# Optimization experiments

Measured on AMD Instinct MI355X. Metric: run time of the kernel, lower is better.

Reference implementation:

```python
import jax, jax.numpy as jnp
import numpy as np

D = 512        # feat_dim
H_ENC = 8      # motion_encoder heads
H_SA = 4       # semantic-aware attention heads
BS, L, N = 8, 512, 4096
LN_EPS = 1e-5


def _layernorm(x, g, b):
    m = jnp.mean(x, axis=-1, keepdims=True)
    v = jnp.var(x, axis=-1, keepdims=True)
    return (x - m) * jax.lax.rsqrt(v + LN_EPS) * g + b


def _linear(x, w, b):
    # torch nn.Linear convention: w [out, in]
    return x @ w.T + b


def setup_inputs() -> dict:
    key = jax.random.key(0)
    ks = jax.random.split(key, 24)
    s = 0.02
    inp = {
        "motion": jax.random.normal(ks[0], (BS, L, D), jnp.float32),
        "scene_xyz": jax.random.normal(ks[1], (BS, N, 3), jnp.float32),
        "scene_feats": jax.random.normal(ks[2], (BS, N, D), jnp.float32),
        "spatial_prior": jax.random.normal(ks[3], (BS, L, N), jnp.float32),
        # motion_encoder (pre-norm MHA + pre-norm MLP, both residual)
        "enc_ln1_g": jnp.ones((D,), jnp.float32),
        "enc_ln1_b": jnp.zeros((D,), jnp.float32),
        "enc_qkv_w": jax.random.normal(ks[4], (3 * D, D), jnp.float32) * s,
        "enc_qkv_b": jnp.zeros((3 * D,), jnp.float32),
        "enc_out_w": jax.random.normal(ks[5], (D, D), jnp.float32) * s,
        "enc_out_b": jnp.zeros((D,), jnp.float32),
        "enc_ln2_g": jnp.ones((D,), jnp.float32),
        "enc_ln2_b": jnp.zeros((D,), jnp.float32),
        "enc_ff1_w": jax.random.normal(ks[6], (D, D), jnp.float32) * s,
        "enc_ff1_b": jnp.zeros((D,), jnp.float32),
        "enc_ff2_w": jax.random.normal(ks[7], (D, D), jnp.float32) * s,
        "enc_ff2_b": jnp.zeros((D,), jnp.float32),
        # SemanticAwareAttention
        "sa_q_w": jax.random.normal(ks[8], (D, D), jnp.float32) * s,
        "sa_q_b": jnp.zeros((D,), jnp.float32),
        "sa_kv_w": jax.random.normal(ks[9], (2 * D, D), jnp.float32) * s,
        "sa_kv_b": jnp.zeros((2 * D,), jnp.float32),
        "sa_out_w": jax.random.normal(ks[10], (D, D), jnp.float32) * s,
        "sa_out_b": jnp.zeros((D,), jnp.float32),
        # final concat-MLP: in 2D -> 4D -> D  (Mlp(2D, D, expansion=4))
        "mlp_fc1_w": jax.random.normal(ks[11], (4 * D, 2 * D), jnp.float32) * s,
        "mlp_fc1_b": jnp.zeros((4 * D,), jnp.float32),
        "mlp_fc2_w": jax.random.normal(ks[12], (D, 4 * D), jnp.float32) * s,
        "mlp_fc2_b": jnp.zeros((D,), jnp.float32),
    }
    return inp


def _forward(motion, scene_xyz, scene_feats, spatial_prior,
             enc_ln1_g, enc_ln1_b, enc_qkv_w, enc_qkv_b, enc_out_w, enc_out_b,
             enc_ln2_g, enc_ln2_b, enc_ff1_w, enc_ff1_b, enc_ff2_w, enc_ff2_b,
             sa_q_w, sa_q_b, sa_kv_w, sa_kv_b, sa_out_w, sa_out_b,
             mlp_fc1_w, mlp_fc1_b, mlp_fc2_w, mlp_fc2_b):
    bs, slen, _ = motion.shape
    n = scene_feats.shape[1]
    dh_enc = D // H_ENC
    dh_sa = D // H_SA

    # ---- motion encoder: pre-norm MHA + residual ----
    h = _layernorm(motion, enc_ln1_g, enc_ln1_b)
    qkv = _linear(h, enc_qkv_w, enc_qkv_b)                      # [bs, L, 3D]
    q, k, v = jnp.split(qkv, 3, axis=-1)
    q = q.reshape(bs, slen, H_ENC, dh_enc)
    k = k.reshape(bs, slen, H_ENC, dh_enc)
    v = v.reshape(bs, slen, H_ENC, dh_enc)
    att = jnp.einsum("bqhd,bkhd->bhqk", q, k) * (dh_enc ** -0.5)
    att = jax.nn.softmax(att, axis=-1)
    o = jnp.einsum("bhqk,bkhd->bqhd", att, v).reshape(bs, slen, D)
    x = motion + _linear(o, enc_out_w, enc_out_b)

    # ---- pre-norm MLP + residual ----
    h2 = _layernorm(x, enc_ln2_g, enc_ln2_b)
    ff = _linear(jax.nn.gelu(_linear(h2, enc_ff1_w, enc_ff1_b), approximate=False),
                 enc_ff2_w, enc_ff2_b)
    motion_sca = x + ff

    # ---- SemanticAwareAttention ----
    q = _linear(motion_sca, sa_q_w, sa_q_b) * (D ** -0.5)       # scale by feat_dim (faithful)
    kv = _linear(scene_feats, sa_kv_w, sa_kv_b)
    k, v = jnp.split(kv, 2, axis=-1)
    # faithful to torch: q.view(bs, H, L, d) splits heads from flattened (L, D)
    q = q.reshape(bs, H_SA, slen, dh_sa)
    k = k.reshape(bs, n, H_SA, dh_sa).transpose(0, 2, 1, 3)     # [bs, H, N, d]
    v = v.reshape(bs, n, H_SA, dh_sa).transpose(0, 2, 1, 3)
    att = jnp.einsum("bhqd,bhkd->bhqk", q, k) + spatial_prior[:, None, :, :]
    att = jax.nn.softmax(att, axis=-1)
    sm = jnp.einsum("bhqk,bhkd->bqhd", att, v).reshape(bs, slen, D)
    sm_feature = _linear(sm, sa_out_w, sa_out_b)

    # ---- concat + MLP ----
    cat = jnp.concatenate([motion_sca, sm_feature], axis=-1)    # [bs, L, 2D]
    out = _linear(jax.nn.gelu(_linear(cat, mlp_fc1_w, mlp_fc1_b), approximate=False),
                  mlp_fc2_w, mlp_fc2_b)
    return out


def reference(motion, scene_xyz, scene_feats, spatial_prior,
              enc_ln1_g, enc_ln1_b, enc_qkv_w, enc_qkv_b, enc_out_w, enc_out_b,
              enc_ln2_g, enc_ln2_b, enc_ff1_w, enc_ff1_b, enc_ff2_w, enc_ff2_b,
              sa_q_w, sa_q_b, sa_kv_w, sa_kv_b, sa_out_w, sa_out_b,
              mlp_fc1_w, mlp_fc1_b, mlp_fc2_w, mlp_fc2_b):
    return _forward(motion, scene_xyz, scene_feats, spatial_prior,
                    enc_ln1_g, enc_ln1_b, enc_qkv_w, enc_qkv_b, enc_out_w, enc_out_b,
                    enc_ln2_g, enc_ln2_b, enc_ff1_w, enc_ff1_b, enc_ff2_w, enc_ff2_b,
                    sa_q_w, sa_q_b, sa_kv_w, sa_kv_b, sa_out_w, sa_out_b,
                    mlp_fc1_w, mlp_fc1_b, mlp_fc2_w, mlp_fc2_b)
```

## Files before the change

### kernel.cpp

```cpp
#include <hip/hip_runtime.h>

typedef unsigned short bf16_t;
typedef __attribute__((ext_vector_type(8))) short bf16x8;
typedef __attribute__((ext_vector_type(4))) float f32x4;

__device__ __forceinline__ float bf2f(bf16_t u) {
  union { unsigned int i; float f; } v; v.i = ((unsigned int)u) << 16; return v.f;
}
__device__ __forceinline__ bf16_t f2bf(float f) {
  union { float f; unsigned int i; } v; v.f = f;
  unsigned int u = v.i;
  u += 0x7fffu + ((u >> 16) & 1u);
  return (bf16_t)(u >> 16);
}
__device__ __forceinline__ float gelu_exact(float x) {
  return 0.5f * x * (1.0f + erff(x * 0.7071067811865475f));
}

__global__ __launch_bounds__(256) void f2bf_kernel(const float4* __restrict__ s,
                                                   ushort4* __restrict__ d, int n4) {
  int i = blockIdx.x * 256 + threadIdx.x;
  if (i < n4) {
    float4 f = s[i];
    ushort4 u; u.x = f2bf(f.x); u.y = f2bf(f.y); u.z = f2bf(f.z); u.w = f2bf(f.w);
    d[i] = u;
  }
}

__global__ __launch_bounds__(256) void ln_kernel(const float* __restrict__ x,
                                                 const float* __restrict__ g,
                                                 const float* __restrict__ bta,
                                                 bf16_t* __restrict__ y) {
  const int w = threadIdx.x >> 6, lane = threadIdx.x & 63;
  const long row = (long)blockIdx.x * 4 + w;
  const long base = row * 512;
  const int c0 = lane << 2;
  float v[8];
  float4 f0 = *(const float4*)(x + base + c0);
  float4 f1 = *(const float4*)(x + base + 256 + c0);
  v[0]=f0.x; v[1]=f0.y; v[2]=f0.z; v[3]=f0.w;
  v[4]=f1.x; v[5]=f1.y; v[6]=f1.z; v[7]=f1.w;
  float s = 0.f;
#pragma unroll
  for (int c=0;c<8;++c) s += v[c];
#pragma unroll
  for (int o=32;o>0;o>>=1) s += __shfl_xor(s, o);
  const float mean = s * 0.001953125f;
  float ss = 0.f;
#pragma unroll
  for (int c=0;c<8;++c) { float d = v[c]-mean; ss += d*d; }
#pragma unroll
  for (int o=32;o>0;o>>=1) ss += __shfl_xor(ss, o);
  const float rstd = rsqrtf(ss * 0.001953125f + 1e-5f);
  ushort4 o0, o1;
  o0.x = f2bf((v[0]-mean)*rstd*g[c0+0] + bta[c0+0]);
  o0.y = f2bf((v[1]-mean)*rstd*g[c0+1] + bta[c0+1]);
  o0.z = f2bf((v[2]-mean)*rstd*g[c0+2] + bta[c0+2]);
  o0.w = f2bf((v[3]-mean)*rstd*g[c0+3] + bta[c0+3]);
  o1.x = f2bf((v[4]-mean)*rstd*g[256+c0+0] + bta[256+c0+0]);
  o1.y = f2bf((v[5]-mean)*rstd*g[256+c0+1] + bta[256+c0+1]);
  o1.z = f2bf((v[6]-mean)*rstd*g[256+c0+2] + bta[256+c0+2]);
  o1.w = f2bf((v[7]-mean)*rstd*g[256+c0+3] + bta[256+c0+3]);
  *(ushort4*)(y + base + c0) = o0;
  *(ushort4*)(y + base + 256 + c0) = o1;
}

struct MmaNT {
  const bf16_t* A; const bf16_t* W; const float* bias; const float* res; void* C;
  long lda, sAb, sAh;
  long ldw, sWb, sWh;
  long ldr, sRb, sRh;
  long ldc, sCb, sCh;
  int K, zdiv, cBf, act;
  float scale;
};

template <int MT>
__global__ __launch_bounds__(256) void mma_nt_kernel(MmaNT p) {
  constexpr int FM = MT / 32;
  __shared__ __align__(16) bf16_t smem[MT * 128];
  const int tid = threadIdx.x;
  const int wid = tid >> 6, lane = tid & 63;
  const int wm = wid & 1, wn = wid >> 1;
  const int quad = lane >> 4, l16 = lane & 15;
  const int z = blockIdx.z;
  const int zb = z / p.zdiv, zh = z % p.zdiv;

  const int nbx = gridDim.x;
  const int nwg = nbx * gridDim.y;
  const int flat = blockIdx.y * nbx + blockIdx.x;
  const int sw = (flat & 7) * (nwg >> 3) + (flat >> 3);
  const int bx = sw % nbx, by = sw / nbx;

  const long m0 = (long)by * MT;
  const long n0 = (long)bx * 128;
  const bf16_t* Ag = p.A + (long)zb * p.sAb + (long)zh * p.sAh +
                     (m0 + wm * (MT / 2) + l16) * p.lda;
  const bf16_t* Wg = p.W + (long)zb * p.sWb + (long)zh * p.sWh +
                     (n0 + wn * 64 + l16) * p.ldw;

  f32x4 zero4 = {0.f, 0.f, 0.f, 0.f};
  f32x4 acc[FM][4];
#pragma unroll
  for (int fm = 0; fm < FM; ++fm)
#pragma unroll
    for (int fn = 0; fn < 4; ++fn) acc[fm][fn] = zero4;

  bf16x8 af[FM], wf[4];
#pragma unroll
  for (int fm = 0; fm < FM; ++fm)
    af[fm] = *(const bf16x8*)(Ag + (long)(fm * 16) * p.lda + quad * 8);
#pragma unroll
  for (int fn = 0; fn < 4; ++fn)
    wf[fn] = *(const bf16x8*)(Wg + (long)(fn * 16) * p.ldw + quad * 8);

  for (int kc = 0; kc < p.K; kc += 32) {
    bf16x8 afn[FM], wfn[4];
    const int kn = kc + 32;
    if (kn < p.K) {
#pragma unroll
      for (int fm = 0; fm < FM; ++fm)
        afn[fm] = *(const bf16x8*)(Ag + (long)(fm * 16) * p.lda + kn + quad * 8);
#pragma unroll
      for (int fn = 0; fn < 4; ++fn)
        wfn[fn] = *(const bf16x8*)(Wg + (long)(fn * 16) * p.ldw + kn + quad * 8);
    }
#pragma unroll
    for (int fm = 0; fm < FM; ++fm)
#pragma unroll
      for (int fn = 0; fn < 4; ++fn)
        acc[fm][fn] = __builtin_amdgcn_mfma_f32_16x16x32_bf16(af[fm], wf[fn], acc[fm][fn], 0, 0, 0);
#pragma unroll
    for (int fm = 0; fm < FM; ++fm) af[fm] = afn[fm];
#pragma unroll
    for (int fn = 0; fn < 4; ++fn) wf[fn] = wfn[fn];
  }

  const long cOff = (long)zb * p.sCb + (long)zh * p.sCh;
  const long rOff = (long)zb * p.sRb + (long)zh * p.sRh;
  if (p.cBf) {
#pragma unroll
    for (int fm = 0; fm < FM; ++fm) {
#pragma unroll
      for (int fn = 0; fn < 4; ++fn) {
        const int lc = wn * 64 + fn * 16 + l16;
        const long col = n0 + lc;
        const float bv = p.bias ? p.bias[col] : 0.f;
#pragma unroll
        for (int r = 0; r < 4; ++r) {
          const int lr = wm * (MT / 2) + fm * 16 + quad * 4 + r;
          float t = acc[fm][fn][r] + bv;
          if (p.act) t = gelu_exact(t);
          t *= p.scale;
          if (p.res) t += p.res[rOff + (m0 + lr) * p.ldr + col];
          smem[lr * 128 + lc] = f2bf(t);
        }
      }
    }
    __syncthreads();
    bf16_t* Cg = (bf16_t*)p.C + cOff + m0 * p.ldc + n0;
#pragma unroll
    for (int i = 0; i < MT / 16; ++i) {
      const int flat2 = tid + i * 256;
      const int r = flat2 >> 4, c = (flat2 & 15) * 8;
      *(uint4*)(Cg + (long)r * p.ldc + c) = *(const uint4*)&smem[r * 128 + c];
    }
  } else {
#pragma unroll
    for (int fm = 0; fm < FM; ++fm) {
#pragma unroll
      for (int fn = 0; fn < 4; ++fn) {
        const long col = n0 + wn * 64 + fn * 16 + l16;
        const float bv = p.bias ? p.bias[col] : 0.f;
#pragma unroll
        for (int r = 0; r < 4; ++r) {
          const long row = m0 + wm * (MT / 2) + fm * 16 + quad * 4 + r;
          float t = acc[fm][fn][r] + bv;
          if (p.act) t = gelu_exact(t);
          t *= p.scale;
          if (p.res) t += p.res[rOff + row * p.ldr + col];
          ((float*)p.C)[cOff + row * p.ldc + col] = t;
        }
      }
    }
  }
}

struct TransP {
  const bf16_t* src; bf16_t* dst;
  long sSb, sSh, ld;
  int nh, N, D;
};

__global__ __launch_bounds__(256) void transpose_kernel(TransP p) {
  __shared__ bf16_t T[64][72];
  const int tid = threadIdx.x;
  const int z = blockIdx.z;
  const int zb = z / p.nh, zh = z % p.nh;
  const long n0 = (long)blockIdx.x * 64;
  const long d0 = (long)blockIdx.y * 64;
  const bf16_t* src = p.src + (long)zb * p.sSb + (long)zh * p.sSh;
  bf16_t* dst = p.dst + (long)z * p.D * p.N;
#pragma unroll
  for (int i = 0; i < 2; ++i) {
    int flat = tid + i * 256, r = flat >> 3, cg = flat & 7;
    uint4 v = *(const uint4*)(src + (n0 + r) * p.ld + d0 + cg * 8);
    *(uint4*)&T[r][cg * 8] = v;
  }
  __syncthreads();
#pragma unroll
  for (int i = 0; i < 2; ++i) {
    int flat = tid + i * 256, dr = flat >> 3, ncg = flat & 7;
    uint4 o;
    unsigned int* op = (unsigned int*)&o;
#pragma unroll
    for (int j = 0; j < 4; ++j)
      op[j] = (unsigned int)T[ncg * 8 + 2 * j][dr] | ((unsigned int)T[ncg * 8 + 2 * j + 1][dr] << 16);
    *(uint4*)(dst + (d0 + dr) * p.N + n0 + ncg * 8) = o;
  }
}

struct FlashP2 {
  const bf16_t* Q; const bf16_t* K; const bf16_t* VT; const float* prior;
  float* partO; float* partML;
  long ldq, sQb, sQh;
  long ldk, sKb, sKh;
  long sVz, sPb;
  int nh, N, segN;
  float scale;
};

template <int DH, int HASP>
__global__ __launch_bounds__(256) void flash3_kernel(FlashP2 p) {
  constexpr int KK = DH / 32;
  constexpr int NFO = DH / 16;
  constexpr int KPAD = DH + 8;
  __shared__ bf16_t Kl[64 * KPAD];
  __shared__ bf16_t Vl[DH * 72];
  __shared__ bf16_t Pl[128 * 72];
  const int tid = threadIdx.x;
  const int w = tid >> 6, lane = tid & 63;
  const int quad = lane >> 4, l16 = lane & 15;
  const int z = blockIdx.z;
  const int zb = z / p.nh, zh = z % p.nh;
  const int qr0 = blockIdx.y * 128 + w * 32;
  const bf16_t* Q = p.Q + (long)zb * p.sQb + (long)zh * p.sQh + (long)qr0 * p.ldq;
  const bf16_t* K = p.K + (long)zb * p.sKb + (long)zh * p.sKh;
  const bf16_t* VT = p.VT + (long)z * p.sVz;

  bf16x8 qf[2][KK];
#pragma unroll
  for (int fm = 0; fm < 2; ++fm)
#pragma unroll
    for (int kk = 0; kk < KK; ++kk)
      qf[fm][kk] = *(const bf16x8*)(Q + (long)(fm * 16 + l16) * p.ldq + kk * 32 + quad * 8);

  f32x4 zero4 = {0.f, 0.f, 0.f, 0.f};
  f32x4 O[2][NFO];
  float m_[2][4], l_[2][4];
#pragma unroll
  for (int fm = 0; fm < 2; ++fm) {
#pragma unroll
    for (int f = 0; f < NFO; ++f) O[fm][f] = zero4;
#pragma unroll
    for (int r = 0; r < 4; ++r) { m_[fm][r] = -1e30f; l_[fm][r] = 0.f; }
  }

  const int k0 = blockIdx.x * p.segN;
  for (int kt = k0; kt < k0 + p.segN; kt += 64) {
    __syncthreads();
    constexpr int KTH = DH / 8;
#pragma unroll
    for (int i = 0; i < DH / 32; ++i) {
      int flat = tid + i * 256, r = flat / KTH, c = (flat % KTH) * 8;
      *(uint4*)&Kl[r * KPAD + c] = *(const uint4*)(K + (long)(kt + r) * p.ldk + c);
    }
#pragma unroll
    for (int i = 0; i < DH / 32; ++i) {
      int flat = tid + i * 256, r = flat >> 3, c = (flat & 7) * 8;
      *(uint4*)&Vl[r * 72 + c] = *(const uint4*)(VT + (long)r * p.N + kt + c);
    }
    float pr[2][4][4];
    if (HASP) {
#pragma unroll
      for (int fm = 0; fm < 2; ++fm) {
        const float* PR = p.prior + (long)zb * p.sPb +
                          (long)(qr0 + fm * 16 + quad * 4) * p.N + kt;
#pragma unroll
        for (int nf = 0; nf < 4; ++nf)
#pragma unroll
          for (int r = 0; r < 4; ++r)
            pr[fm][nf][r] = PR[(long)r * p.N + nf * 16 + l16];
      }
    }
    __syncthreads();
    f32x4 s[2][4];
#pragma unroll
    for (int nf = 0; nf < 4; ++nf) { s[0][nf] = zero4; s[1][nf] = zero4; }
#pragma unroll
    for (int nf = 0; nf < 4; ++nf)
#pragma unroll
      for (int kk = 0; kk < KK; ++kk) {
        bf16x8 kf = *(const bf16x8*)&Kl[(nf * 16 + l16) * KPAD + kk * 32 + quad * 8];
        s[0][nf] = __builtin_amdgcn_mfma_f32_16x16x32_bf16(qf[0][kk], kf, s[0][nf], 0, 0, 0);
        s[1][nf] = __builtin_amdgcn_mfma_f32_16x16x32_bf16(qf[1][kk], kf, s[1][nf], 0, 0, 0);
      }
    float tm[2][4];
#pragma unroll
    for (int fm = 0; fm < 2; ++fm) {
#pragma unroll
      for (int r = 0; r < 4; ++r) tm[fm][r] = -1e30f;
#pragma unroll
      for (int nf = 0; nf < 4; ++nf)
#pragma unroll
        for (int r = 0; r < 4; ++r) {
          float t = s[fm][nf][r] * p.scale;
          if (HASP) t += pr[fm][nf][r];
          s[fm][nf][r] = t;
          tm[fm][r] = fmaxf(tm[fm][r], t);
        }
    }
#pragma unroll
    for (int off = 1; off < 16; off <<= 1)
#pragma unroll
      for (int fm = 0; fm < 2; ++fm)
#pragma unroll
        for (int r = 0; r < 4; ++r) tm[fm][r] = fmaxf(tm[fm][r], __shfl_xor(tm[fm][r], off));
    float alpha[2][4], rs[2][4];
#pragma unroll
    for (int fm = 0; fm < 2; ++fm)
#pragma unroll
      for (int r = 0; r < 4; ++r) {
        float mn = fmaxf(m_[fm][r], tm[fm][r]);
        alpha[fm][r] = __expf(m_[fm][r] - mn);
        m_[fm][r] = mn;
        rs[fm][r] = 0.f;
      }
#pragma unroll
    for (int fm = 0; fm < 2; ++fm)
#pragma unroll
      for (int nf = 0; nf < 4; ++nf)
#pragma unroll
        for (int r = 0; r < 4; ++r) {
          float pv = __expf(s[fm][nf][r] - m_[fm][r]);
          s[fm][nf][r] = pv;
          rs[fm][r] += pv;
        }
#pragma unroll
    for (int off = 1; off < 16; off <<= 1)
#pragma unroll
      for (int fm = 0; fm < 2; ++fm)
#pragma unroll
        for (int r = 0; r < 4; ++r) rs[fm][r] += __shfl_xor(rs[fm][r], off);
#pragma unroll
    for (int fm = 0; fm < 2; ++fm)
#pragma unroll
      for (int r = 0; r < 4; ++r) l_[fm][r] = l_[fm][r] * alpha[fm][r] + rs[fm][r];
#pragma unroll
    for (int fm = 0; fm < 2; ++fm)
#pragma unroll
      for (int nf = 0; nf < 4; ++nf)
#pragma unroll
        for (int r = 0; r < 4; ++r)
          Pl[(w * 32 + fm * 16 + quad * 4 + r) * 72 + nf * 16 + l16] = f2bf(s[fm][nf][r]);
#pragma unroll
    for (int fm = 0; fm < 2; ++fm)
#pragma unroll
      for (int f = 0; f < NFO; ++f)
#pragma unroll
        for (int r = 0; r < 4; ++r) O[fm][f][r] *= alpha[fm][r];
    bf16x8 pf[2][2];
#pragma unroll
    for (int fm = 0; fm < 2; ++fm)
#pragma unroll
      for (int kk2 = 0; kk2 < 2; ++kk2)
        pf[fm][kk2] = *(const bf16x8*)&Pl[(w * 32 + fm * 16 + l16) * 72 + kk2 * 32 + quad * 8];
#pragma unroll
    for (int f = 0; f < NFO; ++f)
#pragma unroll
      for (int kk2 = 0; kk2 < 2; ++kk2) {
        bf16x8 vf = *(const bf16x8*)&Vl[(f * 16 + l16) * 72 + kk2 * 32 + quad * 8];
        O[0][f] = __builtin_amdgcn_mfma_f32_16x16x32_bf16(pf[0][kk2], vf, O[0][f], 0, 0, 0);
        O[1][f] = __builtin_amdgcn_mfma_f32_16x16x32_bf16(pf[1][kk2], vf, O[1][f], 0, 0, 0);
      }
  }
  const long t = ((long)z * gridDim.y + blockIdx.y) * gridDim.x + blockIdx.x;
  float* PO = p.partO + t * (128 * DH);
  float* PM = p.partML + t * 256;
#pragma unroll
  for (int fm = 0; fm < 2; ++fm) {
#pragma unroll
    for (int f = 0; f < NFO; ++f)
#pragma unroll
      for (int r = 0; r < 4; ++r)
        PO[(long)(w * 32 + fm * 16 + quad * 4 + r) * DH + f * 16 + l16] = O[fm][f][r];
    if (l16 == 0) {
#pragma unroll
      for (int r = 0; r < 4; ++r) {
        PM[(w * 32 + fm * 16 + quad * 4 + r) * 2 + 0] = m_[fm][r];
        PM[(w * 32 + fm * 16 + quad * 4 + r) * 2 + 1] = l_[fm][r];
      }
    }
  }
}

struct MergeP {
  const float* partO; const float* partML; bf16_t* C;
  long ldc, sCb;
  int nh, y;
};

template <int DH, int NS>
__global__ __launch_bounds__(256) void fmerge_kernel(MergeP p) {
  const int tid = threadIdx.x;
  const int r = tid >> 1, ch = tid & 1;
  const int blk = blockIdx.x;
  const int z = blk / p.y, qb = blk % p.y;
  const int zb = z / p.nh, zh = z % p.nh;
  const long t0 = (long)blk * NS;
  float mm[NS], wgt[NS];
  float mstar = -1e30f;
#pragma unroll
  for (int s = 0; s < NS; ++s) {
    mm[s] = p.partML[(t0 + s) * 256 + r * 2];
    mstar = fmaxf(mstar, mm[s]);
  }
  float lsum = 0.f;
#pragma unroll
  for (int s = 0; s < NS; ++s) {
    wgt[s] = __expf(mm[s] - mstar);
    lsum += wgt[s] * p.partML[(t0 + s) * 256 + r * 2 + 1];
  }
  const float inv = 1.0f / lsum;
  const int c0 = ch * (DH / 2);
  bf16_t* Cp = p.C + (long)zb * p.sCb + (long)(qb * 128 + r) * p.ldc + (long)zh * DH + c0;
#pragma unroll
  for (int c = 0; c < DH / 2; c += 4) {
    float4 acc = make_float4(0.f, 0.f, 0.f, 0.f);
#pragma unroll
    for (int s = 0; s < NS; ++s) {
      float4 v = *(const float4*)(p.partO + (t0 + s) * (128 * DH) + (long)r * DH + c0 + c);
      acc.x += wgt[s] * v.x; acc.y += wgt[s] * v.y;
      acc.z += wgt[s] * v.z; acc.w += wgt[s] * v.w;
    }
    ushort4 o;
    o.x = f2bf(acc.x * inv); o.y = f2bf(acc.y * inv);
    o.z = f2bf(acc.z * inv); o.w = f2bf(acc.w * inv);
    *(ushort4*)(Cp + c) = o;
  }
}

#define MB(x) ((long)(x) << 20)

extern "C" void kernel_launch(void* const* d_in, const int* in_sizes, int n_in,
                              void* d_out, int out_size, void* d_ws, size_t ws_size,
                              hipStream_t stream) {
  const float* motion      = (const float*)d_in[0];
  const float* scene_feats = (const float*)d_in[2];
  const float* prior       = (const float*)d_in[3];
  const float* ln1_g = (const float*)d_in[4];
  const float* ln1_b = (const float*)d_in[5];
  const float* qkv_w = (const float*)d_in[6];
  const float* qkv_b = (const float*)d_in[7];
  const float* out_w = (const float*)d_in[8];
  const float* out_b = (const float*)d_in[9];
  const float* ln2_g = (const float*)d_in[10];
  const float* ln2_b = (const float*)d_in[11];
  const float* ff1_w = (const float*)d_in[12];
  const float* ff1_b = (const float*)d_in[13];
  const float* ff2_w = (const float*)d_in[14];
  const float* ff2_b = (const float*)d_in[15];
  const float* saq_w = (const float*)d_in[16];
  const float* saq_b = (const float*)d_in[17];
  const float* sakv_w = (const float*)d_in[18];
  const float* sakv_b = (const float*)d_in[19];
  const float* saout_w = (const float*)d_in[20];
  const float* saout_b = (const float*)d_in[21];
  const float* fc1_w = (const float*)d_in[22];
  const float* fc1_b = (const float*)d_in[23];
  const float* fc2_w = (const float*)d_in[24];
  const float* fc2_b = (const float*)d_in[25];

  char* W = (char*)d_ws;
  bf16_t* h_bf    = (bf16_t*)(W + MB(0));
  float*  x_f     = (float*) (W + MB(4));
  bf16_t* o_ff    = (bf16_t*)(W + MB(12));
  bf16_t* qkv_bf  = (bf16_t*)(W + MB(16));
  bf16_t* qsa     = (bf16_t*)(W + MB(28));
  bf16_t* sm_bf   = (bf16_t*)(W + MB(32));
  bf16_t* cat_bf  = (bf16_t*)(W + MB(36));
  bf16_t* fc1g    = (bf16_t*)(W + MB(44));
  bf16_t* vTe     = (bf16_t*)(W + MB(60));
  bf16_t* kv_bf   = (bf16_t*)(W + MB(64));
  bf16_t* vT      = (bf16_t*)(W + MB(128));
  bf16_t* wbase   = (bf16_t*)(W + MB(160));
  bf16_t* scene_bf= (bf16_t*)(W + MB(172));

  float* encO  = (float*)fc1g;
  float* encML = (float*)cat_bf;
  float* saO   = (float*)scene_bf;
  float* saML  = (float*)vTe;

  bf16_t* wq   = wbase + 0L;
  bf16_t* wout = wbase + 786432L;
  bf16_t* wff1 = wbase + 1048576L;
  bf16_t* wff2 = wbase + 1310720L;
  bf16_t* wsaq = wbase + 1572864L;
  bf16_t* wskv = wbase + 1835008L;
  bf16_t* wsout= wbase + 2359296L;
  bf16_t* wfc1 = wbase + 2621440L;
  bf16_t* wfc2 = wbase + 4718592L;

  const dim3 B256(256);
  auto cvt = [&](const float* s, bf16_t* d, long n) {
    int n4 = (int)(n / 4);
    f2bf_kernel<<<(n4 + 255) / 256, B256, 0, stream>>>((const float4*)s, (ushort4*)d, n4);
  };
  cvt(qkv_w,  wq,   786432);
  cvt(out_w,  wout, 262144);
  cvt(ff1_w,  wff1, 262144);
  cvt(ff2_w,  wff2, 262144);
  cvt(saq_w,  wsaq, 262144);
  cvt(sakv_w, wskv, 524288);
  cvt(saout_w,wsout,262144);
  cvt(fc1_w,  wfc1, 2097152);
  cvt(fc2_w,  wfc2, 1048576);
  cvt(scene_feats, scene_bf, 16777216);

  ln_kernel<<<1024, B256, 0, stream>>>(motion, ln1_g, ln1_b, h_bf);

  { MmaNT p{}; p.scale=1.f; p.zdiv=1; p.cBf=1;
    p.A=h_bf; p.lda=512; p.W=wq; p.ldw=512; p.bias=qkv_b;
    p.C=qkv_bf; p.ldc=1536; p.K=512;
    mma_nt_kernel<128><<<dim3(12,32,1), B256, 0, stream>>>(p); }

  { TransP t{}; t.src=qkv_bf+1024; t.dst=vTe; t.sSb=786432; t.sSh=64;
    t.ld=1536; t.nh=8; t.N=512; t.D=64;
    transpose_kernel<<<dim3(8,1,64), B256, 0, stream>>>(t); }
  { FlashP2 p{};
    p.Q=qkv_bf;     p.ldq=1536; p.sQb=786432; p.sQh=64;
    p.K=qkv_bf+512; p.ldk=1536; p.sKb=786432; p.sKh=64;
    p.VT=vTe; p.sVz=32768;
    p.prior=nullptr; p.sPb=0;
    p.partO=encO; p.partML=encML;
    p.nh=8; p.N=512; p.segN=256; p.scale=0.125f;
    flash3_kernel<64,0><<<dim3(2,4,64), B256, 0, stream>>>(p); }
  { MergeP m{}; m.partO=encO; m.partML=encML; m.C=o_ff;
    m.ldc=512; m.sCb=262144; m.nh=8; m.y=4;
    fmerge_kernel<64,2><<<256, B256, 0, stream>>>(m); }

  { MmaNT p{}; p.scale=1.f; p.zdiv=1;
    p.A=o_ff; p.lda=512; p.W=wout; p.ldw=512; p.bias=out_b;
    p.res=motion; p.ldr=512;
    p.C=x_f; p.ldc=512; p.K=512;
    mma_nt_kernel<64><<<dim3(4,64,1), B256, 0, stream>>>(p); }

  ln_kernel<<<1024, B256, 0, stream>>>(x_f, ln2_g, ln2_b, h_bf);

  { MmaNT p{}; p.scale=1.f; p.zdiv=1; p.cBf=1; p.act=1;
    p.A=h_bf; p.lda=512; p.W=wff1; p.ldw=512; p.bias=ff1_b;
    p.C=o_ff; p.ldc=512; p.K=512;
    mma_nt_kernel<64><<<dim3(4,64,1), B256, 0, stream>>>(p); }

  { MmaNT p{}; p.scale=1.f; p.zdiv=1; p.cBf=1;
    p.A=o_ff; p.lda=512; p.W=wff2; p.ldw=512; p.bias=ff2_b;
    p.res=x_f; p.ldr=512;
    p.C=cat_bf; p.ldc=1024; p.K=512;
    mma_nt_kernel<64><<<dim3(4,64,1), B256, 0, stream>>>(p); }

  { MmaNT p{}; p.zdiv=1; p.cBf=1; p.scale=0.04419417382415922f;
    p.A=cat_bf; p.lda=1024; p.W=wsaq; p.ldw=512; p.bias=saq_b;
    p.C=qsa; p.ldc=512; p.K=512;
    mma_nt_kernel<64><<<dim3(4,64,1), B256, 0, stream>>>(p); }

  { MmaNT p{}; p.scale=1.f; p.zdiv=1; p.cBf=1;
    p.A=scene_bf; p.lda=512; p.W=wskv; p.ldw=512; p.bias=sakv_b;
    p.C=kv_bf; p.ldc=1024; p.K=512;
    mma_nt_kernel<128><<<dim3(8,256,1), B256, 0, stream>>>(p); }

  { TransP t{}; t.src=kv_bf+512; t.dst=vT; t.sSb=4194304; t.sSh=128;
    t.ld=1024; t.nh=4; t.N=4096; t.D=128;
    transpose_kernel<<<dim3(64,2,32), B256, 0, stream>>>(t); }
  { FlashP2 p{};
    p.Q=qsa;   p.ldq=128;  p.sQb=262144;  p.sQh=65536;
    p.K=kv_bf; p.ldk=1024; p.sKb=4194304; p.sKh=128;
    p.VT=vT; p.sVz=524288;
    p.prior=prior; p.sPb=2097152;
    p.partO=saO; p.partML=saML;
    p.nh=4; p.N=4096; p.segN=1024; p.scale=1.f;
    flash3_kernel<128,1><<<dim3(4,4,32), B256, 0, stream>>>(p); }
  { MergeP m{}; m.partO=saO; m.partML=saML; m.C=sm_bf;
    m.ldc=512; m.sCb=262144; m.nh=4; m.y=4;
    fmerge_kernel<128,4><<<128, B256, 0, stream>>>(m); }

  { MmaNT p{}; p.scale=1.f; p.zdiv=1; p.cBf=1;
    p.A=sm_bf; p.lda=512; p.W=wsout; p.ldw=512; p.bias=saout_b;
    p.C=cat_bf + 512; p.ldc=1024; p.K=512;
    mma_nt_kernel<64><<<dim3(4,64,1), B256, 0, stream>>>(p); }

  { MmaNT p{}; p.scale=1.f; p.zdiv=1; p.cBf=1; p.act=1;
    p.A=cat_bf; p.lda=1024; p.W=wfc1; p.ldw=1024; p.bias=fc1_b;
    p.C=fc1g; p.ldc=2048; p.K=1024;
    mma_nt_kernel<128><<<dim3(16,32,1), B256, 0, stream>>>(p); }

  { MmaNT p{}; p.scale=1.f; p.zdiv=1;
    p.A=fc1g; p.lda=2048; p.W=wfc2; p.ldw=2048; p.bias=fc2_b;
    p.C=d_out; p.ldc=512; p.K=2048;
    mma_nt_kernel<64><<<dim3(4,64,1), B256, 0, stream>>>(p); }
}
```

Before: 801.6 us.

## Halve flash attention query tile to 64 rows and alias P onto K smem

Each flash block now handles 64 query rows (16 per wave) instead of 128, which doubles the grid in the y dimension and halves the per-thread accumulator and score registers. The P staging buffer now reuses the K shared-memory region, with an extra barrier before P is written, so each block needs less LDS. The merge kernel is retuned to 64-row partials with four threads per row. The intent is higher occupancy and more blocks for the long-sequence semantic-aware attention. The cost is that K/V tiles are loaded once per 64 query rows instead of per 128, doubling K/V traffic, plus one extra sync per iteration.

```diff
diff --git a/kernel.cpp b/kernel.cpp
--- a/kernel.cpp
+++ b/kernel.cpp
@@ -235,36 +235,32 @@
   constexpr int KK = DH / 32;
   constexpr int NFO = DH / 16;
   constexpr int KPAD = DH + 8;
-  __shared__ bf16_t Kl[64 * KPAD];
-  __shared__ bf16_t Vl[DH * 72];
-  __shared__ bf16_t Pl[128 * 72];
+  __shared__ bf16_t smem[64 * KPAD + DH * 72];
+  bf16_t* Kl = smem;
+  bf16_t* Pl = smem;
+  bf16_t* Vl = smem + 64 * KPAD;
   const int tid = threadIdx.x;
   const int w = tid >> 6, lane = tid & 63;
   const int quad = lane >> 4, l16 = lane & 15;
   const int z = blockIdx.z;
   const int zb = z / p.nh, zh = z % p.nh;
-  const int qr0 = blockIdx.y * 128 + w * 32;
+  const int qr0 = blockIdx.y * 64 + w * 16;
   const bf16_t* Q = p.Q + (long)zb * p.sQb + (long)zh * p.sQh + (long)qr0 * p.ldq;
   const bf16_t* K = p.K + (long)zb * p.sKb + (long)zh * p.sKh;
   const bf16_t* VT = p.VT + (long)z * p.sVz;
 
-  bf16x8 qf[2][KK];
-#pragma unroll
-  for (int fm = 0; fm < 2; ++fm)
-#pragma unroll
-    for (int kk = 0; kk < KK; ++kk)
-      qf[fm][kk] = *(const bf16x8*)(Q + (long)(fm * 16 + l16) * p.ldq + kk * 32 + quad * 8);
+  bf16x8 qf[KK];
+#pragma unroll
+  for (int kk = 0; kk < KK; ++kk)
+    qf[kk] = *(const bf16x8*)(Q + (long)l16 * p.ldq + kk * 32 + quad * 8);
 
   f32x4 zero4 = {0.f, 0.f, 0.f, 0.f};
-  f32x4 O[2][NFO];
-  float m_[2][4], l_[2][4];
-#pragma unroll
-  for (int fm = 0; fm < 2; ++fm) {
-#pragma unroll
-    for (int f = 0; f < NFO; ++f) O[fm][f] = zero4;
-#pragma unroll
-    for (int r = 0; r < 4; ++r) { m_[fm][r] = -1e30f; l_[fm][r] = 0.f; }
-  }
+  f32x4 O[NFO];
+  float m_[4], l_[4];
+#pragma unroll
+  for (int f = 0; f < NFO; ++f) O[f] = zero4;
+#pragma unroll
+  for (int r = 0; r < 4; ++r) { m_[r] = -1e30f; l_[r] = 0.f; }
 
   const int k0 = blockIdx.x * p.segN;
   for (int kt = k0; kt < k0 + p.segN; kt += 64) {
@@ -280,126 +276,101 @@
       int flat = tid + i * 256, r = flat >> 3, c = (flat & 7) * 8;
       *(uint4*)&Vl[r * 72 + c] = *(const uint4*)(VT + (long)r * p.N + kt + c);
     }
-    float pr[2][4][4];
+    float pr[4][4];
     if (HASP) {
-#pragma unroll
-      for (int fm = 0; fm < 2; ++fm) {
-        const float* PR = p.prior + (long)zb * p.sPb +
-                          (long)(qr0 + fm * 16 + quad * 4) * p.N + kt;
-#pragma unroll
-        for (int nf = 0; nf < 4; ++nf)
-#pragma unroll
-          for (int r = 0; r < 4; ++r)
-            pr[fm][nf][r] = PR[(long)r * p.N + nf * 16 + l16];
-      }
+      const float* PR = p.prior + (long)zb * p.sPb +
+                        (long)(qr0 + quad * 4) * p.N + kt;
+#pragma unroll
+      for (int nf = 0; nf < 4; ++nf)
+#pragma unroll
+        for (int r = 0; r < 4; ++r)
+          pr[nf][r] = PR[(long)r * p.N + nf * 16 + l16];
     }
     __syncthreads();
-    f32x4 s[2][4];
-#pragma unroll
-    for (int nf = 0; nf < 4; ++nf) { s[0][nf] = zero4; s[1][nf] = zero4; }
+    f32x4 s[4];
+#pragma unroll
+    for (int nf = 0; nf < 4; ++nf) s[nf] = zero4;
 #pragma unroll
     for (int nf = 0; nf < 4; ++nf)
 #pragma unroll
       for (int kk = 0; kk < KK; ++kk) {
         bf16x8 kf = *(const bf16x8*)&Kl[(nf * 16 + l16) * KPAD + kk * 32 + quad * 8];
-        s[0][nf] = __builtin_amdgcn_mfma_f32_16x16x32_bf16(qf[0][kk], kf, s[0][nf], 0, 0, 0);
-        s[1][nf] = __builtin_amdgcn_mfma_f32_16x16x32_bf16(qf[1][kk], kf, s[1][nf], 0, 0, 0);
+        s[nf] = __builtin_amdgcn_mfma_f32_16x16x32_bf16(qf[kk], kf, s[nf], 0, 0, 0);
       }
-    float tm[2][4];
-#pragma unroll
-    for (int fm = 0; fm < 2; ++fm) {
-#pragma unroll
-      for (int r = 0; r < 4; ++r) tm[fm][r] = -1e30f;
-#pragma unroll
-      for (int nf = 0; nf < 4; ++nf)
-#pragma unroll
-        for (int r = 0; r < 4; ++r) {
-          float t = s[fm][nf][r] * p.scale;
-          if (HASP) t += pr[fm][nf][r];
-          s[fm][nf][r] = t;
-          tm[fm][r] = fmaxf(tm[fm][r], t);
-        }
-    }
+    float tm[4];
+#pragma unroll
+    for (int r = 0; r < 4; ++r) tm[r] = -1e30f;
+#pragma unroll
+    for (int nf = 0; nf < 4; ++nf)
+#pragma unroll
+      for (int r = 0; r < 4; ++r) {
+        float t = s[nf][r] * p.scale;
+        if (HASP) t += pr[nf][r];
+        s[nf][r] = t;
+        tm[r] = fmaxf(tm[r], t);
+      }
 #pragma unroll
     for (int off = 1; off < 16; off <<= 1)
 #pragma unroll
-      for (int fm = 0; fm < 2; ++fm)
-#pragma unroll
-        for (int r = 0; r < 4; ++r) tm[fm][r] = fmaxf(tm[fm][r], __shfl_xor(tm[fm][r], off));
-    float alpha[2][4], rs[2][4];
-#pragma unroll
-    for (int fm = 0; fm < 2; ++fm)
+      for (int r = 0; r < 4; ++r) tm[r] = fmaxf(tm[r], __shfl_xor(tm[r], off));
+    float alpha[4], rs[4];
+#pragma unroll
+    for (int r = 0; r < 4; ++r) {
+      float mn = fmaxf(m_[r], tm[r]);
+      alpha[r] = __expf(m_[r] - mn);
+      m_[r] = mn;
+      rs[r] = 0.f;
+    }
+#pragma unroll
+    for (int nf = 0; nf < 4; ++nf)
 #pragma unroll
       for (int r = 0; r < 4; ++r) {
-        float mn = fmaxf(m_[fm][r], tm[fm][r]);
-        alpha[fm][r] = __expf(m_[fm][r] - mn);
-        m_[fm][r] = mn;
-        rs[fm][r] = 0.f;
+        float pv = __expf(s[nf][r] - m_[r]);
+        s[nf][r] = pv;
+        rs[r] += pv;
       }
 #pragma unroll
-    for (int fm = 0; fm < 2; ++fm)
-#pragma unroll
-      for (int nf = 0; nf < 4; ++nf)
-#pragma unroll
-        for (int r = 0; r < 4; ++r) {
-          float pv = __expf(s[fm][nf][r] - m_[fm][r]);
-          s[fm][nf][r] = pv;
-          rs[fm][r] += pv;
-        }
-#pragma unroll
     for (int off = 1; off < 16; off <<= 1)
 #pragma unroll
-      for (int fm = 0; fm < 2; ++fm)
-#pragma unroll
-        for (int r = 0; r < 4; ++r) rs[fm][r] += __shfl_xor(rs[fm][r], off);
-#pragma unroll
-    for (int fm = 0; fm < 2; ++fm)
-#pragma unroll
-      for (int r = 0; r < 4; ++r) l_[fm][r] = l_[fm][r] * alpha[fm][r] + rs[fm][r];
-#pragma unroll
-    for (int fm = 0; fm < 2; ++fm)
-#pragma unroll
-      for (int nf = 0; nf < 4; ++nf)
-#pragma unroll
-        for (int r = 0; r < 4; ++r)
-          Pl[(w * 32 + fm * 16 + quad * 4 + r) * 72 + nf * 16 + l16] = f2bf(s[fm][nf][r]);
-#pragma unroll
-    for (int fm = 0; fm < 2; ++fm)
-#pragma unroll
-      for (int f = 0; f < NFO; ++f)
-#pragma unroll
-        for (int r = 0; r < 4; ++r) O[fm][f][r] *= alpha[fm][r];
-    bf16x8 pf[2][2];
-#pragma unroll
-    for (int fm = 0; fm < 2; ++fm)
-#pragma unroll
-      for (int kk2 = 0; kk2 < 2; ++kk2)
-        pf[fm][kk2] = *(const bf16x8*)&Pl[(w * 32 + fm * 16 + l16) * 72 + kk2 * 32 + quad * 8];
+      for (int r = 0; r < 4; ++r) rs[r] += __shfl_xor(rs[r], off);
+#pragma unroll
+    for (int r = 0; r < 4; ++r) l_[r] = l_[r] * alpha[r] + rs[r];
+    __syncthreads();
+#pragma unroll
+    for (int nf = 0; nf < 4; ++nf)
+#pragma unroll
+      for (int r = 0; r < 4; ++r)
+        Pl[(w * 16 + quad * 4 + r) * 72 + nf * 16 + l16] = f2bf(s[nf][r]);
+#pragma unroll
+    for (int f = 0; f < NFO; ++f)
+#pragma unroll
+      for (int r = 0; r < 4; ++r) O[f][r] *= alpha[r];
+    bf16x8 pf[2];
+#pragma unroll
+    for (int kk2 = 0; kk2 < 2; ++kk2)
+      pf[kk2] = *(const bf16x8*)&Pl[(w * 16 + l16) * 72 + kk2 * 32 + quad * 8];
 #pragma unroll
     for (int f = 0; f < NFO; ++f)
 #pragma unroll
       for (int kk2 = 0; kk2 < 2; ++kk2) {
         bf16x8 vf = *(const bf16x8*)&Vl[(f * 16 + l16) * 72 + kk2 * 32 + quad * 8];
-        O[0][f] = __builtin_amdgcn_mfma_f32_16x16x32_bf16(pf[0][kk2], vf, O[0][f], 0, 0, 0);
-        O[1][f] = __builtin_amdgcn_mfma_f32_16x16x32_bf16(pf[1][kk2], vf, O[1][f], 0, 0, 0);
+        O[f] = __builtin_amdgcn_mfma_f32_16x16x32_bf16(pf[kk2], vf, O[f], 0, 0, 0);
       }
   }
   const long t = ((long)z * gridDim.y + blockIdx.y) * gridDim.x + blockIdx.x;
-  float* PO = p.partO + t * (128 * DH);
-  float* PM = p.partML + t * 256;
-#pragma unroll
-  for (int fm = 0; fm < 2; ++fm) {
-#pragma unroll
-    for (int f = 0; f < NFO; ++f)
-#pragma unroll
-      for (int r = 0; r < 4; ++r)
-        PO[(long)(w * 32 + fm * 16 + quad * 4 + r) * DH + f * 16 + l16] = O[fm][f][r];
-    if (l16 == 0) {
-#pragma unroll
-      for (int r = 0; r < 4; ++r) {
-        PM[(w * 32 + fm * 16 + quad * 4 + r) * 2 + 0] = m_[fm][r];
-        PM[(w * 32 + fm * 16 + quad * 4 + r) * 2 + 1] = l_[fm][r];
-      }
+  float* PO = p.partO + t * (64 * DH);
+  float* PM = p.partML + t * 128;
+  const int row = w * 16 + quad * 4;
+#pragma unroll
+  for (int f = 0; f < NFO; ++f)
+#pragma unroll
+    for (int r = 0; r < 4; ++r)
+      PO[(long)(row + r) * DH + f * 16 + l16] = O[f][r];
+  if (l16 == 0) {
+#pragma unroll
+    for (int r = 0; r < 4; ++r) {
+      PM[(row + r) * 2 + 0] = m_[r];
+      PM[(row + r) * 2 + 1] = l_[r];
     }
   }
 }
@@ -413,7 +384,7 @@
 template <int DH, int NS>
 __global__ __launch_bounds__(256) void fmerge_kernel(MergeP p) {
   const int tid = threadIdx.x;
-  const int r = tid >> 1, ch = tid & 1;
+  const int r = tid >> 2, ch = tid & 3;
   const int blk = blockIdx.x;
   const int z = blk / p.y, qb = blk % p.y;
   const int zb = z / p.nh, zh = z % p.nh;
@@ -422,24 +393,24 @@
   float mstar = -1e30f;
 #pragma unroll
   for (int s = 0; s < NS; ++s) {
-    mm[s] = p.partML[(t0 + s) * 256 + r * 2];
+    mm[s] = p.partML[(t0 + s) * 128 + r * 2];
     mstar = fmaxf(mstar, mm[s]);
   }
   float lsum = 0.f;
 #pragma unroll
   for (int s = 0; s < NS; ++s) {
     wgt[s] = __expf(mm[s] - mstar);
-    lsum += wgt[s] * p.partML[(t0 + s) * 256 + r * 2 + 1];
+    lsum += wgt[s] * p.partML[(t0 + s) * 128 + r * 2 + 1];
   }
   const float inv = 1.0f / lsum;
-  const int c0 = ch * (DH / 2);
-  bf16_t* Cp = p.C + (long)zb * p.sCb + (long)(qb * 128 + r) * p.ldc + (long)zh * DH + c0;
-#pragma unroll
-  for (int c = 0; c < DH / 2; c += 4) {
+  const int c0 = ch * (DH / 4);
+  bf16_t* Cp = p.C + (long)zb * p.sCb + (long)(qb * 64 + r) * p.ldc + (long)zh * DH + c0;
+#pragma unroll
+  for (int c = 0; c < DH / 4; c += 4) {
     float4 acc = make_float4(0.f, 0.f, 0.f, 0.f);
 #pragma unroll
     for (int s = 0; s < NS; ++s) {
-      float4 v = *(const float4*)(p.partO + (t0 + s) * (128 * DH) + (long)r * DH + c0 + c);
+      float4 v = *(const float4*)(p.partO + (t0 + s) * (64 * DH) + (long)r * DH + c0 + c);
       acc.x += wgt[s] * v.x; acc.y += wgt[s] * v.y;
       acc.z += wgt[s] * v.z; acc.w += wgt[s] * v.w;
     }
@@ -544,10 +515,10 @@
     p.prior=nullptr; p.sPb=0;
     p.partO=encO; p.partML=encML;
     p.nh=8; p.N=512; p.segN=256; p.scale=0.125f;
-    flash3_kernel<64,0><<<dim3(2,4,64), B256, 0, stream>>>(p); }
+    flash3_kernel<64,0><<<dim3(2,8,64), B256, 0, stream>>>(p); }
   { MergeP m{}; m.partO=encO; m.partML=encML; m.C=o_ff;
-    m.ldc=512; m.sCb=262144; m.nh=8; m.y=4;
-    fmerge_kernel<64,2><<<256, B256, 0, stream>>>(m); }
+    m.ldc=512; m.sCb=262144; m.nh=8; m.y=8;
+    fmerge_kernel<64,2><<<512, B256, 0, stream>>>(m); }
 
   { MmaNT p{}; p.scale=1.f; p.zdiv=1;
     p.A=o_ff; p.lda=512; p.W=wout; p.ldw=512; p.bias=out_b;
@@ -588,10 +559,10 @@
     p.prior=prior; p.sPb=2097152;
     p.partO=saO; p.partML=saML;
     p.nh=4; p.N=4096; p.segN=1024; p.scale=1.f;
-    flash3_kernel<128,1><<<dim3(4,4,32), B256, 0, stream>>>(p); }
+    flash3_kernel<128,1><<<dim3(4,8,32), B256, 0, stream>>>(p); }
   { MergeP m{}; m.partO=saO; m.partML=saML; m.C=sm_bf;
-    m.ldc=512; m.sCb=262144; m.nh=4; m.y=4;
-    fmerge_kernel<128,4><<<128, B256, 0, stream>>>(m); }
+    m.ldc=512; m.sCb=262144; m.nh=4; m.y=8;
+    fmerge_kernel<128,4><<<256, B256, 0, stream>>>(m); }
 
   { MmaNT p{}; p.scale=1.f; p.zdiv=1; p.cBf=1;
     p.A=sm_bf; p.lda=512; p.W=wsout; p.ldw=512; p.bias=saout_b;
```

After: 796.9 us. Within noise of the previous version (-0.6%).
